# Performance work log

Hardware: AMD Instinct MI355X
Metric: run time of the kernel (lower is better)

The kernel has to match this reference:

```python
import jax, jax.numpy as jnp
import numpy as np

V = 50000  # item vocab (input_size == output_size)
H = 256    # hidden_size
B = 512    # batch_size


def setup_inputs() -> dict:
    key = jax.random.key(0)
    ks = jax.random.split(key, 8)
    return {
        "input_ids": jax.random.randint(ks[0], (B,), 0, V),
        "hidden": jax.random.normal(ks[1], (1, B, H), jnp.float32),
        # GRU layer-0 params, PyTorch layout: gates stacked as [r, z, n]
        "w_ih": jax.random.normal(ks[2], (3 * H, V), jnp.float32) * 0.02,
        "w_hh": jax.random.normal(ks[3], (3 * H, H), jnp.float32) * 0.05,
        "b_ih": jax.random.normal(ks[4], (3 * H,), jnp.float32) * 0.01,
        "b_hh": jax.random.normal(ks[5], (3 * H,), jnp.float32) * 0.01,
        # h2o linear
        "w_out": jax.random.normal(ks[6], (V, H), jnp.float32) * 0.02,
        "b_out": jax.random.normal(ks[7], (V,), jnp.float32) * 0.01,
    }


def _gru_step(one_hot, h0, w_ih, w_hh, b_ih, b_hh):
    # one-hot scatter feeding the input-to-hidden GEMM (as in the torch module)
    gi = one_hot @ w_ih.T + b_ih          # [B, 3H]
    gh = h0 @ w_hh.T + b_hh               # [B, 3H]
    i_r, i_z, i_n = jnp.split(gi, 3, axis=-1)
    h_r, h_z, h_n = jnp.split(gh, 3, axis=-1)
    r = jax.nn.sigmoid(i_r + h_r)
    z = jax.nn.sigmoid(i_z + h_z)
    n = jnp.tanh(i_n + r * h_n)
    return (1.0 - z) * n + z * h0         # [B, H]


def reference(input_ids, hidden, w_ih, w_hh, b_ih, b_hh, w_out, b_out):
    # onehot_encode: zero buffer + scatter 1.0 at item index
    one_hot = jnp.zeros((B, V), w_ih.dtype).at[jnp.arange(B), input_ids].set(1.0)
    h1 = _gru_step(one_hot, hidden[0], w_ih, w_hh, b_ih, b_hh)  # [B, H]
    logit = jnp.tanh(h1 @ w_out.T + b_out)                      # final_activation = Tanh
    return logit, h1[None]  # ([B, V], [1, B, H])
```

## Files before the change

### kernel.cpp

```cpp
#include <hip/hip_runtime.h>
#include <hip/hip_bf16.h>

#define V 50000
#define H 256
#define B 512

typedef __bf16 bf16x8 __attribute__((ext_vector_type(8)));
typedef float f32x4 __attribute__((ext_vector_type(4)));

__device__ __forceinline__ float tanh_fast(float x) {
    float a = __builtin_fabsf(x);
    float e = __expf(2.0f * a);
    float r = fmaf(-2.0f, __builtin_amdgcn_rcpf(e + 1.0f), 1.0f);
    return __builtin_copysignf(r, x);
}

__global__ __launch_bounds__(256) void gru_h1_kernel(
    const int* __restrict__ ids, const float* __restrict__ h0,
    const float* __restrict__ w_ih, const float* __restrict__ w_hh,
    const float* __restrict__ b_ih, const float* __restrict__ b_hh,
    float* __restrict__ h1_out, __bf16* __restrict__ h1b)
{
    __shared__ float h0s[2 * 256];
    const int t = threadIdx.x;
    const int b0 = blockIdx.x * 2;

#pragma unroll
    for (int i = 0; i < 2; i++)
        h0s[i * 256 + t] = h0[(b0 + i) * 256 + t];
    __syncthreads();

    const int j = t;

    int id[2];
    float gir[2], giz[2], gin[2];
#pragma unroll
    for (int m = 0; m < 2; m++) {
        id[m] = ids[b0 + m];
        gir[m] = w_ih[(size_t)j * V + id[m]];
        giz[m] = w_ih[(size_t)(H + j) * V + id[m]];
        gin[m] = w_ih[(size_t)(2 * H + j) * V + id[m]];
    }

    float ar[2] = {0.f, 0.f}, az[2] = {0.f, 0.f}, an[2] = {0.f, 0.f};
    const float* __restrict__ wr_p = w_hh + (size_t)j * H;
    const float* __restrict__ wz_p = w_hh + (size_t)(H + j) * H;
    const float* __restrict__ wn_p = w_hh + (size_t)(2 * H + j) * H;

#pragma unroll 4
    for (int k = 0; k < H; k += 4) {
        f32x4 wr = *(const f32x4*)(wr_p + k);
        f32x4 wz = *(const f32x4*)(wz_p + k);
        f32x4 wn = *(const f32x4*)(wn_p + k);
#pragma unroll
        for (int m = 0; m < 2; m++) {
            f32x4 h = *(const f32x4*)&h0s[m * 256 + k];
#pragma unroll
            for (int u = 0; u < 4; u++) {
                ar[m] = fmaf(wr[u], h[u], ar[m]);
                az[m] = fmaf(wz[u], h[u], az[m]);
                an[m] = fmaf(wn[u], h[u], an[m]);
            }
        }
    }

    const float bir = b_ih[j], biz = b_ih[H + j], bin = b_ih[2 * H + j];
    const float bhr = b_hh[j], bhz = b_hh[H + j], bhn = b_hh[2 * H + j];

#pragma unroll
    for (int m = 0; m < 2; m++) {
        float r = 1.f / (1.f + __expf(-(gir[m] + bir + ar[m] + bhr)));
        float z = 1.f / (1.f + __expf(-(giz[m] + biz + az[m] + bhz)));
        float n = tanh_fast(gin[m] + bin + an[m] + bhn * r + r * an[m] * 0.f
                            + r * (an[m] * 0.f));
        n = tanh_fast(gin[m] + bin + r * (an[m] + bhn));
        float h1 = (1.f - z) * n + z * h0s[m * 256 + j];
        h1_out[(b0 + m) * H + j] = h1;
        h1b[(b0 + m) * H + j] = (__bf16)h1;
    }
}

#define BN 64
#define BSTR 264

__global__ __launch_bounds__(256, 4) void logit_kernel(
    const __bf16* __restrict__ h1b, const float* __restrict__ w_out,
    const float* __restrict__ b_out, float* __restrict__ out)
{
    __shared__ __bf16 Bs[BN * BSTR];
    const int t = threadIdx.x;
    const int n0 = blockIdx.x * BN;
    const int m_tile = blockIdx.y;

    {
        const int c4 = t & 63;
        const int v0 = t >> 6;
#pragma unroll
        for (int half = 0; half < 2; half++) {
            f32x4 g[8];
#pragma unroll
            for (int i = 0; i < 8; i++) {
                int n = n0 + v0 + (half * 8 + i) * 4;
                g[i] = (f32x4){0.f, 0.f, 0.f, 0.f};
                if (n < V) g[i] = *(const f32x4*)(w_out + (size_t)n * H + c4 * 4);
            }
#pragma unroll
            for (int i = 0; i < 8; i++) {
                int v = v0 + (half * 8 + i) * 4;
                struct alignas(8) BH4 { __bf16 h[4]; } p;
                p.h[0] = (__bf16)g[i][0];
                p.h[1] = (__bf16)g[i][1];
                p.h[2] = (__bf16)g[i][2];
                p.h[3] = (__bf16)g[i][3];
                *(BH4*)&Bs[v * BSTR + c4 * 4] = p;
            }
        }
    }
    __syncthreads();

    const int lane = t & 63;
    const int wave = t >> 6;
    const int q = lane >> 4;
    const int v16 = lane & 15;
    const int m_base = m_tile * 256 + wave * 64;

    f32x4 acc[4][4];
#pragma unroll
    for (int i = 0; i < 4; i++)
#pragma unroll
        for (int jj = 0; jj < 4; jj++) acc[i][jj] = (f32x4){0.f, 0.f, 0.f, 0.f};

    const __bf16* a_base = h1b + (m_base + v16) * H + q * 8;

#pragma unroll
    for (int ks = 0; ks < 8; ks++) {
        bf16x8 a[4];
#pragma unroll
        for (int i = 0; i < 4; i++)
            a[i] = *(const bf16x8*)(a_base + i * 16 * H + ks * 32);
#pragma unroll
        for (int jj = 0; jj < 4; jj++) {
            bf16x8 bfr = *(const bf16x8*)&Bs[(jj * 16 + v16) * BSTR + ks * 32 + q * 8];
#pragma unroll
            for (int i = 0; i < 4; i++)
                acc[i][jj] = __builtin_amdgcn_mfma_f32_16x16x32_bf16(
                    bfr, a[i], acc[i][jj], 0, 0, 0);
        }
    }

#pragma unroll
    for (int jj = 0; jj < 4; jj++) {
        const int n = n0 + jj * 16 + q * 4;
        if (n < V) {
            f32x4 bo = *(const f32x4*)&b_out[n];
#pragma unroll
            for (int i = 0; i < 4; i++) {
                f32x4 r;
#pragma unroll
                for (int u = 0; u < 4; u++)
                    r[u] = tanh_fast(acc[i][jj][u] + bo[u]);
                *(f32x4*)&out[(size_t)(m_base + i * 16 + v16) * V + n] = r;
            }
        }
    }
}

extern "C" void kernel_launch(void* const* d_in, const int* in_sizes, int n_in,
                              void* d_out, int out_size, void* d_ws, size_t ws_size,
                              hipStream_t stream) {
    const int* ids = (const int*)d_in[0];
    const float* hidden = (const float*)d_in[1];
    const float* w_ih = (const float*)d_in[2];
    const float* w_hh = (const float*)d_in[3];
    const float* b_ih = (const float*)d_in[4];
    const float* b_hh = (const float*)d_in[5];
    const float* w_out = (const float*)d_in[6];
    const float* b_out = (const float*)d_in[7];

    float* out = (float*)d_out;
    float* h1_out = out + (size_t)B * V;
    __bf16* h1b = (__bf16*)d_ws;

    gru_h1_kernel<<<256, 256, 0, stream>>>(ids, hidden, w_ih, w_hh, b_ih, b_hh,
                                           h1_out, h1b);

    dim3 grid((V + BN - 1) / BN, 2);
    logit_kernel<<<grid, 256, 0, stream>>>(h1b, w_out, b_out, out);
}
```

Before: 334.0 us.

## Keep w_out fragments in registers per wave and drop LDS staging in logit kernel

The logit kernel no longer stages a 64-row w_out tile in shared memory. Each wave now loads its own 16 vocab rows straight into bf16 MFMA fragments held in registers, and iterates over 16 batch subtiles while reading h1 fragments from global/L2. This removes the LDS writes, the block barrier and the LDS fragment reads. In exchange, h1b is re-read many more times from cache, register pressure rises with a 16-entry accumulator array, and occupancy drops to 3 blocks per CU. A redundant tanh computation in the GRU kernel is also removed.

```diff
diff --git a/kernel.cpp b/kernel.cpp
--- a/kernel.cpp
+++ b/kernel.cpp
@@ -71,96 +71,71 @@
     for (int m = 0; m < 2; m++) {
         float r = 1.f / (1.f + __expf(-(gir[m] + bir + ar[m] + bhr)));
         float z = 1.f / (1.f + __expf(-(giz[m] + biz + az[m] + bhz)));
-        float n = tanh_fast(gin[m] + bin + an[m] + bhn * r + r * an[m] * 0.f
-                            + r * (an[m] * 0.f));
-        n = tanh_fast(gin[m] + bin + r * (an[m] + bhn));
+        float n = tanh_fast(gin[m] + bin + r * (an[m] + bhn));
         float h1 = (1.f - z) * n + z * h0s[m * 256 + j];
         h1_out[(b0 + m) * H + j] = h1;
         h1b[(b0 + m) * H + j] = (__bf16)h1;
     }
 }
 
-#define BN 64
-#define BSTR 264
-
-__global__ __launch_bounds__(256, 4) void logit_kernel(
+__global__ __launch_bounds__(256, 3) void logit_kernel(
     const __bf16* __restrict__ h1b, const float* __restrict__ w_out,
     const float* __restrict__ b_out, float* __restrict__ out)
 {
-    __shared__ __bf16 Bs[BN * BSTR];
     const int t = threadIdx.x;
-    const int n0 = blockIdx.x * BN;
-    const int m_tile = blockIdx.y;
-
-    {
-        const int c4 = t & 63;
-        const int v0 = t >> 6;
-#pragma unroll
-        for (int half = 0; half < 2; half++) {
-            f32x4 g[8];
-#pragma unroll
-            for (int i = 0; i < 8; i++) {
-                int n = n0 + v0 + (half * 8 + i) * 4;
-                g[i] = (f32x4){0.f, 0.f, 0.f, 0.f};
-                if (n < V) g[i] = *(const f32x4*)(w_out + (size_t)n * H + c4 * 4);
-            }
-#pragma unroll
-            for (int i = 0; i < 8; i++) {
-                int v = v0 + (half * 8 + i) * 4;
-                struct alignas(8) BH4 { __bf16 h[4]; } p;
-                p.h[0] = (__bf16)g[i][0];
-                p.h[1] = (__bf16)g[i][1];
-                p.h[2] = (__bf16)g[i][2];
-                p.h[3] = (__bf16)g[i][3];
-                *(BH4*)&Bs[v * BSTR + c4 * 4] = p;
-            }
-        }
-    }
-    __syncthreads();
-
     const int lane = t & 63;
     const int wave = t >> 6;
     const int q = lane >> 4;
     const int v16 = lane & 15;
-    const int m_base = m_tile * 256 + wave * 64;
+    const int slab = blockIdx.x * 64 + wave * 16;
+    const int n_row = slab + v16;
+    const int m0 = blockIdx.y * 256;
 
-    f32x4 acc[4][4];
+    bf16x8 bfr[8];
+    {
+        const float* bp = w_out + (size_t)n_row * H + q * 8;
+        const bool valid = (n_row < V);
 #pragma unroll
-    for (int i = 0; i < 4; i++)
-#pragma unroll
-        for (int jj = 0; jj < 4; jj++) acc[i][jj] = (f32x4){0.f, 0.f, 0.f, 0.f};
-
-    const __bf16* a_base = h1b + (m_base + v16) * H + q * 8;
-
-#pragma unroll
-    for (int ks = 0; ks < 8; ks++) {
-        bf16x8 a[4];
-#pragma unroll
-        for (int i = 0; i < 4; i++)
-            a[i] = *(const bf16x8*)(a_base + i * 16 * H + ks * 32);
-#pragma unroll
-        for (int jj = 0; jj < 4; jj++) {
-            bf16x8 bfr = *(const bf16x8*)&Bs[(jj * 16 + v16) * BSTR + ks * 32 + q * 8];
-#pragma unroll
-            for (int i = 0; i < 4; i++)
-                acc[i][jj] = __builtin_amdgcn_mfma_f32_16x16x32_bf16(
-                    bfr, a[i], acc[i][jj], 0, 0, 0);
+        for (int ks = 0; ks < 8; ks++) {
+            f32x4 lo = valid ? *(const f32x4*)(bp + ks * 32)     : (f32x4){0.f,0.f,0.f,0.f};
+            f32x4 hi = valid ? *(const f32x4*)(bp + ks * 32 + 4) : (f32x4){0.f,0.f,0.f,0.f};
+            bf16x8 v;
+            v[0] = (__bf16)lo[0]; v[1] = (__bf16)lo[1];
+            v[2] = (__bf16)lo[2]; v[3] = (__bf16)lo[3];
+            v[4] = (__bf16)hi[0]; v[5] = (__bf16)hi[1];
+            v[6] = (__bf16)hi[2]; v[7] = (__bf16)hi[3];
+            bfr[ks] = v;
         }
     }
 
+    const __bf16* ap = h1b + (size_t)(m0 + v16) * H + q * 8;
+
+    f32x4 acc[16];
 #pragma unroll
-    for (int jj = 0; jj < 4; jj++) {
-        const int n = n0 + jj * 16 + q * 4;
-        if (n < V) {
-            f32x4 bo = *(const f32x4*)&b_out[n];
+    for (int mi = 0; mi < 16; mi++) acc[mi] = (f32x4){0.f, 0.f, 0.f, 0.f};
+
 #pragma unroll
-            for (int i = 0; i < 4; i++) {
-                f32x4 r;
+    for (int mi = 0; mi < 16; mi++) {
+        bf16x8 a[8];
 #pragma unroll
-                for (int u = 0; u < 4; u++)
-                    r[u] = tanh_fast(acc[i][jj][u] + bo[u]);
-                *(f32x4*)&out[(size_t)(m_base + i * 16 + v16) * V + n] = r;
-            }
+        for (int ks = 0; ks < 8; ks++)
+            a[ks] = *(const bf16x8*)(ap + mi * 16 * H + ks * 32);
+#pragma unroll
+        for (int ks = 0; ks < 8; ks++)
+            acc[mi] = __builtin_amdgcn_mfma_f32_16x16x32_bf16(
+                bfr[ks], a[ks], acc[mi], 0, 0, 0);
+    }
+
+    const int n_st = slab + q * 4;
+    if (n_st < V) {
+        f32x4 bo = *(const f32x4*)&b_out[n_st];
+#pragma unroll
+        for (int mi = 0; mi < 16; mi++) {
+            f32x4 r;
+#pragma unroll
+            for (int u = 0; u < 4; u++)
+                r[u] = tanh_fast(acc[mi][u] + bo[u]);
+            *(f32x4*)&out[(size_t)(m0 + mi * 16 + v16) * V + n_st] = r;
         }
     }
 }
@@ -184,6 +159,6 @@
     gru_h1_kernel<<<256, 256, 0, stream>>>(ids, hidden, w_ih, w_hh, b_ih, b_hh,
                                            h1_out, h1b);
 
-    dim3 grid((V + BN - 1) / BN, 2);
+    dim3 grid((V + 63) / 64, 2);
     logit_kernel<<<grid, 256, 0, stream>>>(h1b, w_out, b_out, out);
 }
```

New measurement: 393.0 us. +17.7%, slower.
